# Performance work log

Hardware: AMD Instinct MI355X
Metric: run time of the kernel (lower is better)

The kernel has to match this reference:

```python
import jax, jax.numpy as jnp
import numpy as np

K = 7  # kernel_size = (1, 7): horizontal cyclic shifts


@jax.custom_vjp
def binarize(x):
    # BinaryQuantizer: sign forward, clipped STE backward
    return jnp.sign(x)

def _bin_fwd(x):
    return jnp.sign(x), x

def _bin_bwd(x, g):
    # torch zeroes grad where x >= 1 or x <= -1
    return (jnp.where((x > -1.0) & (x < 1.0), g, 0.0),)

binarize.defvjp(_bin_fwd, _bin_bwd)


def setup_inputs() -> dict:
    key = jax.random.key(0)
    k1, k2, k3 = jax.random.split(key, 3)
    B, C, H, W = 32, 384, 56, 56
    x = jax.random.normal(k1, (B, C, H, W), dtype=jnp.float32)
    # weight is (out_channels, in_channels) for the 1x1 conv (squeezed kh=kw=1)
    weight = jax.random.normal(k2, (C, C), dtype=jnp.float32) * 0.05
    bias = jax.random.normal(k3, (C,), dtype=jnp.float32) * 0.01
    return {"x": x, "weight": weight, "bias": bias}


def reference(x, weight, bias):
    B, C, H, W = x.shape
    xb = binarize(x)            # sign(activations)
    wb = binarize(weight)       # sign(weights)

    # CycleFC offsets for kernel (1, K): per-channel integer horizontal shift.
    # dx_i = (i + K*1//2) % K - K//2  (gen_offset with start_idx = K//2)
    dx = (jnp.arange(C) + K // 2) % K - K // 2  # (C,) in [-K//2, K-1-K//2]

    # deform_conv2d with integer offsets == zero-padded shift:
    # shifted[b, i, h, w] = xb[b, i, h, w + dx_i], 0 if out of bounds.
    P = K
    xp = jnp.pad(xb, ((0, 0), (0, 0), (0, 0), (P, P)))
    idx = jnp.arange(W)[None, :] + dx[:, None] + P          # (C, W)
    shifted = jnp.take_along_axis(xp, idx[None, :, None, :], axis=3)  # (B,C,H,W)

    # 1x1 conv (pointwise GEMM) + bias
    out = jnp.einsum('bchw,oc->bohw', shifted, wb) + bias[None, :, None, None]
    return out
```

## Files before the change

kernel.cpp:

```cpp
#include <hip/hip_runtime.h>
#include <stdint.h>

#define B_   32
#define C_   384
#define H_   56
#define W_   56
#define HW_  (H_*W_)
#define NP_  (B_*H_*W_)
#define NWORD 6
#define PIXBLK 392


struct Masks {
    unsigned long long inv[7][NWORD];
    int nvalid[7];
};
constexpr Masks make_masks() {
    Masks m{};
    int wv[7] = {0, 1, 2, 3, 53, 54, 55};
    for (int p = 0; p < 7; ++p) {
        int nv = 0;
        for (int c = 0; c < C_; ++c) {
            int dx = (c + 3) % 7 - 3;
            int wp = wv[p] + dx;
            if (wp >= 0 && wp < W_) nv++;
            else m.inv[p][c >> 6] |= 1ull << (c & 63);
        }
        m.nvalid[p] = nv;
    }
    return m;
}
__device__ constexpr Masks MK = make_masks();

struct InvW { unsigned long long m[W_][NWORD]; };
constexpr InvW make_invw() {
    InvW t{};
    for (int w = 0; w < W_; ++w)
        for (int c = 0; c < C_; ++c) {
            int dx = (c + 3) % 7 - 3;
            int wp = w + dx;
            if (!(wp >= 0 && wp < W_)) t.m[w][c >> 6] |= 1ull << (c & 63);
        }
    return t;
}
__device__ constexpr InvW IVW = make_invw();

__global__ __launch_bounds__(64) void prep_kernel(
        const float* __restrict__ weight, const float* __restrict__ bias,
        unsigned long long* __restrict__ pw, float* __restrict__ C2) {
    int o = blockIdx.x;
    int lane = threadIdx.x;
    unsigned long long words[NWORD];
#pragma unroll
    for (int k = 0; k < NWORD; ++k) {
        float v = weight[o * C_ + k * 64 + lane];
        words[k] = __ballot(v < 0.0f);
    }
    if (lane < NWORD) pw[o * NWORD + lane] = words[lane];
    if (lane < 7) {
        int wb = 0;
#pragma unroll
        for (int k = 0; k < NWORD; ++k)
            wb += __popcll(words[k] & MK.inv[lane][k]);
        C2[o * 7 + lane] = (float)(MK.nvalid[lane] + 2 * wb) + bias[o];
    }
}

template <int K>
__device__ __forceinline__ unsigned long long pack_word(
        const float* __restrict__ xb, int w) {
    constexpr int dxt[7] = {0, 1, 2, 3, -3, -2, -1};
    unsigned long long bits = 0;
#pragma unroll
    for (int j = 0; j < 64; ++j) {
        int dx = dxt[(K * 64 + j) % 7];
        int wp = w + dx;
        int wpc = wp < 0 ? 0 : (wp > W_ - 1 ? W_ - 1 : wp);
        unsigned u = __float_as_uint(
            __builtin_nontemporal_load(&xb[(size_t)j * HW_ + wpc]));
        bits |= (unsigned long long)(u >> 31) << j;
    }
    return bits & ~IVW.m[w][K];
}

__global__ __launch_bounds__(256) void pack_kernel(
        const float* __restrict__ x, unsigned long long* __restrict__ pk) {
    int k = blockIdx.x / PIXBLK;
    unsigned p = (blockIdx.x % PIXBLK) * 256u + threadIdx.x;
    unsigned b = p / (unsigned)HW_;
    unsigned r = p % (unsigned)HW_;
    unsigned h = r / (unsigned)W_;
    int w = (int)(r % (unsigned)W_);

    const float* xb = x + ((size_t)b * C_ + k * 64) * HW_ + h * W_;

    unsigned long long bits;
    switch (k) {
        case 0: bits = pack_word<0>(xb, w); break;
        case 1: bits = pack_word<1>(xb, w); break;
        case 2: bits = pack_word<2>(xb, w); break;
        case 3: bits = pack_word<3>(xb, w); break;
        case 4: bits = pack_word<4>(xb, w); break;
        default: bits = pack_word<5>(xb, w); break;
    }
    pk[(size_t)k * NP_ + p] = bits;
}

__global__ __launch_bounds__(256) void bgemm_kernel(
        const unsigned long long* __restrict__ pk,
        const unsigned long long* __restrict__ pw,
        const float* __restrict__ C2,
        float* __restrict__ out) {
    int oc = blockIdx.x / PIXBLK;
    unsigned p = (blockIdx.x % PIXBLK) * 256u + threadIdx.x;
    unsigned b = p / (unsigned)HW_;
    unsigned w = p % (unsigned)W_;
    int pat = (w < 3u) ? (int)w : ((w >= 53u) ? (int)w - 49 : 3);

    unsigned long long xw[NWORD];
#pragma unroll
    for (int k = 0; k < NWORD; ++k)
        xw[k] = pk[(size_t)k * NP_ + p];

    float* op = out + p + (size_t)b * (C_ - 1) * HW_;

    const int obase = oc * (C_ / 8);
#pragma unroll 4
    for (int oi = 0; oi < C_ / 8; ++oi) {
        int o = obase + oi;
        const unsigned long long* wr = pw + o * NWORD;
        int U = 0;
#pragma unroll
        for (int k = 0; k < NWORD; ++k)
            U += __popcll(xw[k] ^ wr[k]);
        float v = C2[o * 7 + pat] - 2.0f * (float)U;
        __builtin_nontemporal_store(v, &op[(size_t)o * HW_]);
    }
}

__global__ __launch_bounds__(256) void cyclefc_fb_kernel(
        const float* __restrict__ x,
        const unsigned long long* __restrict__ pw,
        const float* __restrict__ C2,
        float* __restrict__ out) {
    unsigned p = blockIdx.x * 256u + threadIdx.x;
    unsigned w = p % (unsigned)W_;
    unsigned bh = p / (unsigned)W_;
    unsigned h = bh % (unsigned)H_;
    unsigned b = bh / (unsigned)H_;
    const float* xb = x + (size_t)b * C_ * HW_ + h * W_;

    constexpr int dxt[7] = {0, 1, 2, 3, -3, -2, -1};
    unsigned long long xw[NWORD];
#pragma unroll
    for (int k = 0; k < NWORD; ++k) {
        unsigned long long bits = 0;
#pragma unroll
        for (int j = 0; j < 64; ++j) {
            int dx = dxt[(k * 64 + j) % 7];
            int wp = (int)w + dx;
            int wpc = wp < 0 ? 0 : (wp > W_ - 1 ? W_ - 1 : wp);
            unsigned u = __float_as_uint(xb[(size_t)(k * 64 + j) * HW_ + wpc]);
            bits |= (unsigned long long)(u >> 31) << j;
        }
        xw[k] = bits & ~IVW.m[w][k];
    }
    int pat = (w < 3u) ? (int)w : ((w >= 53u) ? (int)w - 49 : 3);
    float* op = out + (size_t)b * C_ * HW_ + h * W_ + w;
#pragma unroll 4
    for (int o = 0; o < C_; ++o) {
        const unsigned long long* wr = pw + o * NWORD;
        int U = 0;
#pragma unroll
        for (int k = 0; k < NWORD; ++k)
            U += __popcll(xw[k] ^ wr[k]);
        op[(size_t)o * HW_] = C2[o * 7 + pat] - 2.0f * (float)U;
    }
}

extern "C" void kernel_launch(void* const* d_in, const int* in_sizes, int n_in,
                              void* d_out, int out_size, void* d_ws, size_t ws_size,
                              hipStream_t stream) {
    const float* x      = (const float*)d_in[0];
    const float* weight = (const float*)d_in[1];
    const float* bias   = (const float*)d_in[2];
    float* out = (float*)d_out;

    unsigned long long* pw = (unsigned long long*)d_ws;
    float* C2 = (float*)((char*)d_ws + C_ * NWORD * sizeof(unsigned long long));
    unsigned long long* pk = (unsigned long long*)((char*)d_ws + 32768);
    const size_t need = 32768 + (size_t)NWORD * NP_ * sizeof(unsigned long long);

    prep_kernel<<<dim3(C_), dim3(64), 0, stream>>>(weight, bias, pw, C2);

    if (ws_size >= need) {
        pack_kernel<<<dim3(PIXBLK * NWORD), dim3(256), 0, stream>>>(x, pk);
        bgemm_kernel<<<dim3(PIXBLK * 8), dim3(256), 0, stream>>>(pk, pw, C2, out);
    } else {
        cyclefc_fb_kernel<<<dim3(NP_ / 256), dim3(256), 0, stream>>>(x, pw, C2, out);
    }
}
```

Measured before the change: 273.6 us.

## Fuse bit-packing and binary GEMM into one kernel via shared memory

Replaces the separate pack and bgemm kernels with one kernel per (batch,row) block. Six waves each pack one 64-channel word into shared memory, then each wave computes 64 output channels for the 56 pixels. This removes the global round-trip of the packed activation buffer and one launch. In exchange, 8 of every 64 lanes sit idle, the grid is smaller (1792 blocks), and the old workspace fallback path is dropped.

```diff
diff --git a/kernel.cpp b/kernel.cpp
--- a/kernel.cpp
+++ b/kernel.cpp
@@ -6,9 +6,7 @@
 #define H_   56
 #define W_   56
 #define HW_  (H_*W_)
-#define NP_  (B_*H_*W_)
 #define NWORD 6
-#define PIXBLK 392
 
 
 struct Masks {
@@ -83,50 +81,46 @@
     return bits & ~IVW.m[w][K];
 }
 
-__global__ __launch_bounds__(256) void pack_kernel(
-        const float* __restrict__ x, unsigned long long* __restrict__ pk) {
-    int k = blockIdx.x / PIXBLK;
-    unsigned p = (blockIdx.x % PIXBLK) * 256u + threadIdx.x;
-    unsigned b = p / (unsigned)HW_;
-    unsigned r = p % (unsigned)HW_;
-    unsigned h = r / (unsigned)W_;
-    int w = (int)(r % (unsigned)W_);
-
-    const float* xb = x + ((size_t)b * C_ + k * 64) * HW_ + h * W_;
-
-    unsigned long long bits;
-    switch (k) {
-        case 0: bits = pack_word<0>(xb, w); break;
-        case 1: bits = pack_word<1>(xb, w); break;
-        case 2: bits = pack_word<2>(xb, w); break;
-        case 3: bits = pack_word<3>(xb, w); break;
-        case 4: bits = pack_word<4>(xb, w); break;
-        default: bits = pack_word<5>(xb, w); break;
-    }
-    pk[(size_t)k * NP_ + p] = bits;
-}
-
-__global__ __launch_bounds__(256) void bgemm_kernel(
-        const unsigned long long* __restrict__ pk,
+__global__ __launch_bounds__(384) void fused_kernel(
+        const float* __restrict__ x,
         const unsigned long long* __restrict__ pw,
         const float* __restrict__ C2,
         float* __restrict__ out) {
-    int oc = blockIdx.x / PIXBLK;
-    unsigned p = (blockIdx.x % PIXBLK) * 256u + threadIdx.x;
-    unsigned b = p / (unsigned)HW_;
-    unsigned w = p % (unsigned)W_;
-    int pat = (w < 3u) ? (int)w : ((w >= 53u) ? (int)w - 49 : 3);
+    __shared__ unsigned long long xs[NWORD][W_];
 
+    int b = blockIdx.x / H_;
+    int h = blockIdx.x % H_;
+    int wid  = threadIdx.x >> 6;
+    int lane = threadIdx.x & 63;
+
+    if (lane < W_) {
+        const float* xb = x + ((size_t)b * C_ + wid * 64) * HW_ + h * W_;
+        unsigned long long bits;
+        switch (wid) {
+            case 0: bits = pack_word<0>(xb, lane); break;
+            case 1: bits = pack_word<1>(xb, lane); break;
+            case 2: bits = pack_word<2>(xb, lane); break;
+            case 3: bits = pack_word<3>(xb, lane); break;
+            case 4: bits = pack_word<4>(xb, lane); break;
+            default: bits = pack_word<5>(xb, lane); break;
+        }
+        xs[wid][lane] = bits;
+    }
+    __syncthreads();
+    if (lane >= W_) return;
+
+    int w = lane;
     unsigned long long xw[NWORD];
 #pragma unroll
     for (int k = 0; k < NWORD; ++k)
-        xw[k] = pk[(size_t)k * NP_ + p];
+        xw[k] = xs[k][w];
 
-    float* op = out + p + (size_t)b * (C_ - 1) * HW_;
+    int pat = (w < 3) ? w : ((w >= 53) ? w - 49 : 3);
+    const int obase = wid * 64;
+    float* op = out + ((size_t)b * C_ + obase) * HW_ + (size_t)h * W_ + w;
 
-    const int obase = oc * (C_ / 8);
 #pragma unroll 4
-    for (int oi = 0; oi < C_ / 8; ++oi) {
+    for (int oi = 0; oi < 64; ++oi) {
         int o = obase + oi;
         const unsigned long long* wr = pw + o * NWORD;
         int U = 0;
@@ -134,47 +128,7 @@
         for (int k = 0; k < NWORD; ++k)
             U += __popcll(xw[k] ^ wr[k]);
         float v = C2[o * 7 + pat] - 2.0f * (float)U;
-        __builtin_nontemporal_store(v, &op[(size_t)o * HW_]);
-    }
-}
-
-__global__ __launch_bounds__(256) void cyclefc_fb_kernel(
-        const float* __restrict__ x,
-        const unsigned long long* __restrict__ pw,
-        const float* __restrict__ C2,
-        float* __restrict__ out) {
-    unsigned p = blockIdx.x * 256u + threadIdx.x;
-    unsigned w = p % (unsigned)W_;
-    unsigned bh = p / (unsigned)W_;
-    unsigned h = bh % (unsigned)H_;
-    unsigned b = bh / (unsigned)H_;
-    const float* xb = x + (size_t)b * C_ * HW_ + h * W_;
-
-    constexpr int dxt[7] = {0, 1, 2, 3, -3, -2, -1};
-    unsigned long long xw[NWORD];
-#pragma unroll
-    for (int k = 0; k < NWORD; ++k) {
-        unsigned long long bits = 0;
-#pragma unroll
-        for (int j = 0; j < 64; ++j) {
-            int dx = dxt[(k * 64 + j) % 7];
-            int wp = (int)w + dx;
-            int wpc = wp < 0 ? 0 : (wp > W_ - 1 ? W_ - 1 : wp);
-            unsigned u = __float_as_uint(xb[(size_t)(k * 64 + j) * HW_ + wpc]);
-            bits |= (unsigned long long)(u >> 31) << j;
-        }
-        xw[k] = bits & ~IVW.m[w][k];
-    }
-    int pat = (w < 3u) ? (int)w : ((w >= 53u) ? (int)w - 49 : 3);
-    float* op = out + (size_t)b * C_ * HW_ + h * W_ + w;
-#pragma unroll 4
-    for (int o = 0; o < C_; ++o) {
-        const unsigned long long* wr = pw + o * NWORD;
-        int U = 0;
-#pragma unroll
-        for (int k = 0; k < NWORD; ++k)
-            U += __popcll(xw[k] ^ wr[k]);
-        op[(size_t)o * HW_] = C2[o * 7 + pat] - 2.0f * (float)U;
+        __builtin_nontemporal_store(v, &op[(size_t)oi * HW_]);
     }
 }
 
@@ -188,15 +142,7 @@
 
     unsigned long long* pw = (unsigned long long*)d_ws;
     float* C2 = (float*)((char*)d_ws + C_ * NWORD * sizeof(unsigned long long));
-    unsigned long long* pk = (unsigned long long*)((char*)d_ws + 32768);
-    const size_t need = 32768 + (size_t)NWORD * NP_ * sizeof(unsigned long long);
 
     prep_kernel<<<dim3(C_), dim3(64), 0, stream>>>(weight, bias, pw, C2);
-
-    if (ws_size >= need) {
-        pack_kernel<<<dim3(PIXBLK * NWORD), dim3(256), 0, stream>>>(x, pk);
-        bgemm_kernel<<<dim3(PIXBLK * 8), dim3(256), 0, stream>>>(pk, pw, C2, out);
-    } else {
-        cyclefc_fb_kernel<<<dim3(NP_ / 256), dim3(256), 0, stream>>>(x, pw, C2, out);
-    }
+    fused_kernel<<<dim3(B_ * H_), dim3(384), 0, stream>>>(x, pw, C2, out);
 }
```

Result: slower. 331.5 us (+21.2%).

## Restructure pack and binary GEMM kernels around per-image blocks with register tiling

Applied to the files above, without the earlier changes.

The pack kernel now runs one block per (image, 32-channel half-word) with 512 threads, each handling seven pixels and writing 32-bit halves of the packed 64-bit words. The binary GEMM kernel now assigns each block one image and 24 output channels. Each thread keeps packed activations for three pixels in registers so every weight-word load is reused across several pixels. The aim is more memory-level parallelism in packing and less redundant weight and C2 loading in the GEMM, at the cost of higher register pressure and a ragged tail where only 64 threads do the last pixel group.

```diff
diff --git a/kernel.cpp b/kernel.cpp
--- a/kernel.cpp
+++ b/kernel.cpp
@@ -8,11 +8,17 @@
 #define HW_  (H_*W_)
 #define NP_  (B_*H_*W_)
 #define NWORD 6
-#define PIXBLK 392
+#define TPB  512
+#define NIT  7
+#define OQ   24
+#define NOB  (C_/OQ)
+
+typedef unsigned long long u64;
+typedef unsigned u32;
 
 
 struct Masks {
-    unsigned long long inv[7][NWORD];
+    u64 inv[7][NWORD];
     int nvalid[7];
 };
 constexpr Masks make_masks() {
@@ -32,7 +38,22 @@
 }
 __device__ constexpr Masks MK = make_masks();
 
-struct InvW { unsigned long long m[W_][NWORD]; };
+struct InvW32 { u32 m[W_][12]; };
+constexpr InvW32 make_invw32() {
+    InvW32 t{};
+    for (int w = 0; w < W_; ++w)
+        for (int kh = 0; kh < 12; ++kh)
+            for (int j = 0; j < 32; ++j) {
+                int c = kh * 32 + j;
+                int dx = (c + 3) % 7 - 3;
+                int wp = w + dx;
+                if (!(wp >= 0 && wp < W_)) t.m[w][kh] |= 1u << j;
+            }
+    return t;
+}
+__device__ constexpr InvW32 IVW32 = make_invw32();
+
+struct InvW { u64 m[W_][NWORD]; };
 constexpr InvW make_invw() {
     InvW t{};
     for (int w = 0; w < W_; ++w)
@@ -47,10 +68,10 @@
 
 __global__ __launch_bounds__(64) void prep_kernel(
         const float* __restrict__ weight, const float* __restrict__ bias,
-        unsigned long long* __restrict__ pw, float* __restrict__ C2) {
+        u64* __restrict__ pw, float* __restrict__ C2) {
     int o = blockIdx.x;
     int lane = threadIdx.x;
-    unsigned long long words[NWORD];
+    u64 words[NWORD];
 #pragma unroll
     for (int k = 0; k < NWORD; ++k) {
         float v = weight[o * C_ + k * 64 + lane];
@@ -66,81 +87,122 @@
     }
 }
 
-template <int K>
-__device__ __forceinline__ unsigned long long pack_word(
-        const float* __restrict__ xb, int w) {
+template <int KH>
+__device__ __forceinline__ void pack_body(
+        const float* __restrict__ x, u32* __restrict__ pkw, int b) {
     constexpr int dxt[7] = {0, 1, 2, 3, -3, -2, -1};
-    unsigned long long bits = 0;
-#pragma unroll
-    for (int j = 0; j < 64; ++j) {
-        int dx = dxt[(K * 64 + j) % 7];
-        int wp = w + dx;
-        int wpc = wp < 0 ? 0 : (wp > W_ - 1 ? W_ - 1 : wp);
-        unsigned u = __float_as_uint(
-            __builtin_nontemporal_load(&xb[(size_t)j * HW_ + wpc]));
-        bits |= (unsigned long long)(u >> 31) << j;
-    }
-    return bits & ~IVW.m[w][K];
-}
-
-__global__ __launch_bounds__(256) void pack_kernel(
-        const float* __restrict__ x, unsigned long long* __restrict__ pk) {
-    int k = blockIdx.x / PIXBLK;
-    unsigned p = (blockIdx.x % PIXBLK) * 256u + threadIdx.x;
-    unsigned b = p / (unsigned)HW_;
-    unsigned r = p % (unsigned)HW_;
-    unsigned h = r / (unsigned)W_;
-    int w = (int)(r % (unsigned)W_);
-
-    const float* xb = x + ((size_t)b * C_ + k * 64) * HW_ + h * W_;
-
-    unsigned long long bits;
-    switch (k) {
-        case 0: bits = pack_word<0>(xb, w); break;
-        case 1: bits = pack_word<1>(xb, w); break;
-        case 2: bits = pack_word<2>(xb, w); break;
-        case 3: bits = pack_word<3>(xb, w); break;
-        case 4: bits = pack_word<4>(xb, w); break;
-        default: bits = pack_word<5>(xb, w); break;
-    }
-    pk[(size_t)k * NP_ + p] = bits;
-}
-
-__global__ __launch_bounds__(256) void bgemm_kernel(
-        const unsigned long long* __restrict__ pk,
-        const unsigned long long* __restrict__ pw,
-        const float* __restrict__ C2,
-        float* __restrict__ out) {
-    int oc = blockIdx.x / PIXBLK;
-    unsigned p = (blockIdx.x % PIXBLK) * 256u + threadIdx.x;
-    unsigned b = p / (unsigned)HW_;
-    unsigned w = p % (unsigned)W_;
-    int pat = (w < 3u) ? (int)w : ((w >= 53u) ? (int)w - 49 : 3);
-
-    unsigned long long xw[NWORD];
-#pragma unroll
-    for (int k = 0; k < NWORD; ++k)
-        xw[k] = pk[(size_t)k * NP_ + p];
-
-    float* op = out + p + (size_t)b * (C_ - 1) * HW_;
-
-    const int obase = oc * (C_ / 8);
+    const int tid = threadIdx.x;
+
+    int w_[NIT], rb_[NIT];
+    u32 bits[NIT];
+#pragma unroll
+    for (int it = 0; it < NIT; ++it) {
+        int px = tid + it * TPB;
+        if (px > HW_ - 1) px = HW_ - 1;
+        int w = px % W_;
+        w_[it] = w;
+        rb_[it] = px - w;
+        bits[it] = 0;
+    }
+
+    const float* xb = x + ((size_t)b * C_ + KH * 32) * HW_;
+#pragma unroll
+    for (int j = 0; j < 32; ++j) {
+        const int dx = dxt[(KH * 32 + j) % 7];
+        const float* pb = xb + (size_t)j * HW_;
+#pragma unroll
+        for (int it = 0; it < NIT; ++it) {
+            int wp = w_[it] + dx;
+            int wc = wp < 0 ? 0 : (wp > W_ - 1 ? W_ - 1 : wp);
+            u32 u = __float_as_uint(
+                __builtin_nontemporal_load(&pb[rb_[it] + wc]));
+            bits[it] |= (u >> 31) << j;
+        }
+    }
+
+    const size_t base = (size_t)(KH >> 1) * NP_ + (size_t)b * HW_;
+#pragma unroll
+    for (int it = 0; it < NIT; ++it) {
+        if (it < 6 || tid < 64) {
+            int px = tid + it * TPB;
+            u32 v = bits[it] & ~IVW32.m[w_[it]][KH];
+            pkw[((base + px) << 1) + (KH & 1)] = v;
+        }
+    }
+}
+
+__global__ __launch_bounds__(TPB) void pack_kernel(
+        const float* __restrict__ x, u32* __restrict__ pkw) {
+    const int b  = blockIdx.x / 12;
+    const int kh = blockIdx.x % 12;
+    switch (kh) {
+        case 0:  pack_body<0>(x, pkw, b);  break;
+        case 1:  pack_body<1>(x, pkw, b);  break;
+        case 2:  pack_body<2>(x, pkw, b);  break;
+        case 3:  pack_body<3>(x, pkw, b);  break;
+        case 4:  pack_body<4>(x, pkw, b);  break;
+        case 5:  pack_body<5>(x, pkw, b);  break;
+        case 6:  pack_body<6>(x, pkw, b);  break;
+        case 7:  pack_body<7>(x, pkw, b);  break;
+        case 8:  pack_body<8>(x, pkw, b);  break;
+        case 9:  pack_body<9>(x, pkw, b);  break;
+        case 10: pack_body<10>(x, pkw, b); break;
+        default: pack_body<11>(x, pkw, b); break;
+    }
+}
+
+template <int M>
+__device__ __forceinline__ void bgemm_group(
+        const u64* __restrict__ pk, const u64* __restrict__ pw,
+        const float* __restrict__ C2, float* __restrict__ outb,
+        int obase, int b, int it0) {
+    const int tid = threadIdx.x;
+    const size_t bhw = (size_t)b * HW_;
+
+    int px[M], pat[M];
+    u64 xw[M][NWORD];
+#pragma unroll
+    for (int m = 0; m < M; ++m) {
+        px[m] = tid + (it0 + m) * TPB;
+        int w = px[m] % W_;
+        pat[m] = (w < 3) ? w : ((w >= 53) ? w - 49 : 3);
+#pragma unroll
+        for (int k = 0; k < NWORD; ++k)
+            xw[m][k] = pk[(size_t)k * NP_ + bhw + px[m]];
+    }
+
 #pragma unroll 4
-    for (int oi = 0; oi < C_ / 8; ++oi) {
-        int o = obase + oi;
-        const unsigned long long* wr = pw + o * NWORD;
-        int U = 0;
-#pragma unroll
-        for (int k = 0; k < NWORD; ++k)
-            U += __popcll(xw[k] ^ wr[k]);
-        float v = C2[o * 7 + pat] - 2.0f * (float)U;
-        __builtin_nontemporal_store(v, &op[(size_t)o * HW_]);
-    }
+    for (int oi = 0; oi < OQ; ++oi) {
+        const int o = obase + oi;
+        const u64* wr = pw + o * NWORD;
+#pragma unroll
+        for (int m = 0; m < M; ++m) {
+            int U = 0;
+#pragma unroll
+            for (int k = 0; k < NWORD; ++k)
+                U += __popcll(xw[m][k] ^ wr[k]);
+            float v = C2[o * 7 + pat[m]] - 2.0f * (float)U;
+            __builtin_nontemporal_store(v, &outb[(size_t)o * HW_ + px[m]]);
+        }
+    }
+}
+
+__global__ __launch_bounds__(TPB) void bgemm_kernel(
+        const u64* __restrict__ pk, const u64* __restrict__ pw,
+        const float* __restrict__ C2, float* __restrict__ out) {
+    const int b     = blockIdx.x / NOB;
+    const int obase = (blockIdx.x % NOB) * OQ;
+    float* outb = out + (size_t)b * C_ * HW_;
+
+    bgemm_group<3>(pk, pw, C2, outb, obase, b, 0);
+    bgemm_group<3>(pk, pw, C2, outb, obase, b, 3);
+    if (threadIdx.x < 64)
+        bgemm_group<1>(pk, pw, C2, outb, obase, b, 6);
 }
 
 __global__ __launch_bounds__(256) void cyclefc_fb_kernel(
         const float* __restrict__ x,
-        const unsigned long long* __restrict__ pw,
+        const u64* __restrict__ pw,
         const float* __restrict__ C2,
         float* __restrict__ out) {
     unsigned p = blockIdx.x * 256u + threadIdx.x;
@@ -151,17 +213,17 @@
     const float* xb = x + (size_t)b * C_ * HW_ + h * W_;
 
     constexpr int dxt[7] = {0, 1, 2, 3, -3, -2, -1};
-    unsigned long long xw[NWORD];
+    u64 xw[NWORD];
 #pragma unroll
     for (int k = 0; k < NWORD; ++k) {
-        unsigned long long bits = 0;
+        u64 bits = 0;
 #pragma unroll
         for (int j = 0; j < 64; ++j) {
             int dx = dxt[(k * 64 + j) % 7];
             int wp = (int)w + dx;
             int wpc = wp < 0 ? 0 : (wp > W_ - 1 ? W_ - 1 : wp);
             unsigned u = __float_as_uint(xb[(size_t)(k * 64 + j) * HW_ + wpc]);
-            bits |= (unsigned long long)(u >> 31) << j;
+            bits |= (u64)(u >> 31) << j;
         }
         xw[k] = bits & ~IVW.m[w][k];
     }
@@ -169,7 +231,7 @@
     float* op = out + (size_t)b * C_ * HW_ + h * W_ + w;
 #pragma unroll 4
     for (int o = 0; o < C_; ++o) {
-        const unsigned long long* wr = pw + o * NWORD;
+        const u64* wr = pw + o * NWORD;
         int U = 0;
 #pragma unroll
         for (int k = 0; k < NWORD; ++k)
@@ -186,16 +248,16 @@
     const float* bias   = (const float*)d_in[2];
     float* out = (float*)d_out;
 
-    unsigned long long* pw = (unsigned long long*)d_ws;
-    float* C2 = (float*)((char*)d_ws + C_ * NWORD * sizeof(unsigned long long));
-    unsigned long long* pk = (unsigned long long*)((char*)d_ws + 32768);
-    const size_t need = 32768 + (size_t)NWORD * NP_ * sizeof(unsigned long long);
+    u64* pw = (u64*)d_ws;
+    float* C2 = (float*)((char*)d_ws + C_ * NWORD * sizeof(u64));
+    u64* pk = (u64*)((char*)d_ws + 32768);
+    const size_t need = 32768 + (size_t)NWORD * NP_ * sizeof(u64);
 
     prep_kernel<<<dim3(C_), dim3(64), 0, stream>>>(weight, bias, pw, C2);
 
     if (ws_size >= need) {
-        pack_kernel<<<dim3(PIXBLK * NWORD), dim3(256), 0, stream>>>(x, pk);
-        bgemm_kernel<<<dim3(PIXBLK * 8), dim3(256), 0, stream>>>(pk, pw, C2, out);
+        pack_kernel<<<dim3(B_ * 12), dim3(TPB), 0, stream>>>(x, (u32*)pk);
+        bgemm_kernel<<<dim3(B_ * NOB), dim3(TPB), 0, stream>>>(pk, pw, C2, out);
     } else {
         cyclefc_fb_kernel<<<dim3(NP_ / 256), dim3(256), 0, stream>>>(x, pw, C2, out);
     }
```

New measurement: 306.0 us. 1.12x slower.
